# Kernel tuning notes

Hardware: AMD Instinct MI355X
Metric: run time of the kernel (lower is better)

Reference implementation:

```python
import jax, jax.numpy as jnp
import numpy as np

TOLX = 1e-12
TOLFUN = 1e-06
MAXITER = 1000
ALPHA = 1e-4
MIN_LAMBDA = 0.1
MAX_LAMBDA = 0.5
MAX_STEPS = 10  # fixed unroll budget; Newton converges in < 10 iterations for this problem
BS, NY = 200000, 8


def setup_inputs():
    key = jax.random.key(0)
    k1, k2, k3 = jax.random.split(key, 3)
    y0 = jax.random.normal(k1, (BS, NY), dtype=jnp.float32)
    W = 0.1 * jax.random.normal(k2, (NY, NY), dtype=jnp.float32)
    V = 0.1 * jax.random.normal(k3, (NY, NY), dtype=jnp.float32)
    dt = jnp.asarray(0.1, dtype=jnp.float32)
    t = jnp.asarray(1.0, dtype=jnp.float32)
    return {"y0": y0, "dt": dt, "t": t, "W": W, "V": V}


def _safe_div(n, d, eps=1e-30):
    ok = jnp.abs(d) > eps
    return jnp.where(ok, n / jnp.where(ok, d, 1.0), 0.0)


def _solver(y0, dt, t, W, V):
    bs, ny = y0.shape
    one = jnp.float32(1.0)

    def delta_S(tt, y):
        # test ODE right-hand side g(t, y): mildly nonlinear, acts per-sample
        return jnp.tanh(y @ W) @ V - 0.1 * y + 0.01 * jnp.sin(tt)

    def err(y):  # implicit-Euler residual, (bs, ny)
        return (y - y0) / dt - delta_S(t, y)

    def _err_single(yb, y0b):
        return (yb - y0b) / dt - (jnp.tanh(yb @ W) @ V - 0.1 * yb + 0.01 * jnp.sin(t))

    def batched_jac(y):
        # (bs, ny, ny): d err_b / d y_b; matches torch batch-diagonal of autograd jacobian
        return jax.vmap(jax.jacfwd(_err_single), in_axes=(0, 0))(y, y0)

    F0 = err(y0)
    jac0 = batched_jac(y0)
    rn0 = jnp.max(jnp.abs(F0), axis=1)
    fobj0 = jnp.einsum('bi,bi->b', F0, F0)

    state0 = dict(y=y0, yold=y0, F=F0, dy=jnp.zeros_like(y0), jac=jac0,
                  resnorm=rn0, resnorm0=100.0 * rn0,
                  lam=one, lam1=one, lam2=jnp.float32(0.5),
                  fold=fobj0, f2=fobj0, slope=jnp.zeros((bs,), y0.dtype),
                  lam_min=jnp.float32(0.0), niter=jnp.int32(0), exitflag=jnp.int32(1))

    def body(s, _):
        active = (((jnp.max(s['resnorm']) > TOLFUN) | (s['lam'] < 1.0))
                  & (s['exitflag'] >= 0) & (s['niter'] <= MAXITER))

        # --- lam == 1: fresh Newton direction, slope, objective ---
        is_newton = s['lam'] == 1.0
        recompute = jnp.max(_safe_div(s['resnorm'], s['resnorm0'])) > 0.2
        fresh_jac = batched_jac(s['y'])
        jac = jnp.where(is_newton & recompute, fresh_jac, s['jac'])
        dy_n = -jnp.linalg.solve(jac, s['F'][..., None])[..., 0]  # lstsq on square == solve
        gvec = jnp.einsum('bi,bij->bj', s['F'], jac)
        slope_n = jnp.einsum('bj,bj->b', gvec, dy_n)
        fold_n = jnp.einsum('bi,bi->b', s['F'], s['F'])
        lam_min_n = _safe_div(jnp.float32(TOLX),
                              jnp.max(jnp.abs(dy_n) / jnp.maximum(jnp.abs(s['y']), 1.0)))

        dy = jnp.where(is_newton, dy_n, s['dy'])
        slope = jnp.where(is_newton, slope_n, s['slope'])
        fold = jnp.where(is_newton, fold_n, s['fold'])
        yold = jnp.where(is_newton, s['y'], s['yold'])
        lam_min = jnp.where(is_newton, lam_min_n, s['lam_min'])
        niter = jnp.where(is_newton, s['niter'] + 1, s['niter'])

        brk = s['lam'] < lam_min            # -> exitflag = 2, freeze state
        bad = ~jnp.all(jnp.isfinite(dy))    # -> exitflag = -1, freeze state

        # --- trial step + trust-region line search ---
        lam = s['lam']
        y_new = yold + dy * lam
        F_new = err(y_new)
        f_obj = jnp.einsum('bi,bi->b', F_new, F_new)
        lam1 = lam
        lam2, f2 = s['lam2'], s['f2']

        backtrack = jnp.any(f_obj > fold + ALPHA * lam * slope)
        # quadratic model (first backtrack)
        lam_quad = jnp.min(_safe_div(-slope / 2.0, f_obj - fold - slope))
        # cubic model (subsequent backtracks)
        A = _safe_div(one, lam1 - lam2)
        inv1 = _safe_div(one, lam1 * lam1)
        inv2 = _safe_div(one, lam2 * lam2)
        B = jnp.stack([jnp.stack([inv1, -inv2]), jnp.stack([-lam2 * inv1, lam1 * inv2])])
        C = jnp.stack([f_obj - fold - lam1 * slope, f2 - fold - lam2 * slope])  # (2, bs)
        ab = A * (B @ C)
        a, b = ab[0], ab[1]
        disc = b * b - 3.0 * a * slope
        sq = jnp.sqrt(jnp.maximum(disc, 0.0))
        lam_tmp = jnp.where(jnp.all(a == 0.0), _safe_div(-slope, 2.0 * b),
                   jnp.where(jnp.any(disc < 0.0), MAX_LAMBDA * lam1,
                    jnp.where(jnp.any(b <= 0.0), _safe_div(-b + sq, 3.0 * a),
                     _safe_div(-slope, b + sq))))
        lam_cubic = jnp.min(jnp.minimum(lam_tmp, MAX_LAMBDA * lam1))
        lam_bt = jnp.where(lam == 1.0, lam_quad, lam_cubic)
        nanf = ~jnp.all(jnp.isfinite(f_obj))
        lam_new = jnp.where(backtrack, lam_bt, jnp.where(nanf, MAX_LAMBDA * lam1, one))

        cont = lam_new < 1.0  # retry with smaller lambda next iteration (the `continue` path)
        lam2_new = jnp.where(cont, lam1, lam2)
        f2_new = jnp.where(cont, f_obj, f2)
        lam_new = jnp.where(cont, jnp.maximum(lam_new, MIN_LAMBDA * lam1), lam_new)
        resnorm_new = jnp.where(cont, s['resnorm'], jnp.max(jnp.abs(F_new), axis=1))
        resnorm0_new = jnp.where(cont, s['resnorm0'], s['resnorm'])

        upd = active & (~brk) & (~bad)
        exitflag = jnp.where(active & brk, jnp.int32(2),
                    jnp.where(active & (~brk) & bad, jnp.int32(-1), s['exitflag']))
        sel = lambda new, old: jnp.where(upd, new, old)

        ns = dict(y=sel(y_new, s['y']), yold=sel(yold, s['yold']), F=sel(F_new, s['F']),
                  dy=sel(dy, s['dy']), jac=sel(jac, s['jac']),
                  resnorm=sel(resnorm_new, s['resnorm']), resnorm0=sel(resnorm0_new, s['resnorm0']),
                  lam=sel(lam_new, s['lam']), lam1=sel(lam1, s['lam1']), lam2=sel(lam2_new, s['lam2']),
                  fold=sel(fold, s['fold']), f2=sel(f2_new, s['f2']), slope=sel(slope, s['slope']),
                  lam_min=sel(lam_min, s['lam_min']),
                  niter=jnp.where(active, niter, s['niter']), exitflag=exitflag)
        return ns, None

    sN, _ = jax.lax.scan(body, state0, None, length=MAX_STEPS)
    return sN['y'], sN['F'], sN['exitflag']


def reference(y0, dt, t, W, V):
    y, F, exitflag = _solver(y0, dt, t, W, V)
    return (y, F, exitflag)
```

## Files before the change

### kernel.cpp

```cpp
#include <hip/hip_runtime.h>

#define BSZ 200000
#define NSTEPS 10
#define TOLFUN_C 1e-6f
#define ALPHA_C 1e-4f

#define OFF_Y     ((size_t)0)
#define OFF_YOLD  ((size_t)BSZ*8)
#define OFF_F     ((size_t)BSZ*16)
#define OFF_DY    ((size_t)BSZ*24)
#define OFF_SJ    ((size_t)BSZ*32)
#define OFF_FOLD  ((size_t)BSZ*40)
#define OFF_SLOPE ((size_t)BSZ*41)
#define OFF_RESN  ((size_t)BSZ*42)
#define OFF_F2    ((size_t)BSZ*43)
#define OFF_TRN   ((size_t)BSZ*44)
#define OFF_TFO   ((size_t)BSZ*45)
#define OFF_R     ((size_t)BSZ*46)

#define RSTRIDE 64
#define NSLOT   9
#define R_TOT   (2 + NSTEPS*NSLOT)
#define KEY_MAX_IDENT 0x007FFFFFu
#define KEY_MIN_IDENT 0xFF800000u

static __device__ __forceinline__ float nanmax2(float a, float b){
    return (__builtin_isnan(a) || __builtin_isnan(b)) ? __builtin_nanf("") : fmaxf(a, b);
}
static __device__ __forceinline__ float nanmin2(float a, float b){
    return (__builtin_isnan(a) || __builtin_isnan(b)) ? __builtin_nanf("") : fminf(a, b);
}
static __device__ __forceinline__ float safe_div(float n, float d){
    return (fabsf(d) > 1e-30f) ? (n / d) : 0.0f;
}
static __device__ __forceinline__ unsigned fkey(float x){
    unsigned u = __float_as_uint(x);
    return (u & 0x80000000u) ? ~u : (u | 0x80000000u);
}
static __device__ __forceinline__ float funkey(unsigned u){
    return (u & 0x80000000u) ? __uint_as_float(u & 0x7FFFFFFFu) : __uint_as_float(~u);
}
static __device__ __forceinline__ unsigned fkey_max(float x){
    if (__builtin_isnan(x)) x = __uint_as_float(0x7FC00000u);
    return fkey(x);
}
static __device__ __forceinline__ unsigned fkey_min(float x){
    if (__builtin_isnan(x)) x = __uint_as_float(0xFFC00000u);
    return fkey(x);
}
static __device__ __forceinline__ void ld8(const float* p, float* v){
    float4 a = ((const float4*)p)[0], b = ((const float4*)p)[1];
    v[0]=a.x; v[1]=a.y; v[2]=a.z; v[3]=a.w; v[4]=b.x; v[5]=b.y; v[6]=b.z; v[7]=b.w;
}
static __device__ __forceinline__ void st8(float* p, const float* v){
    float4 a, b;
    a.x=v[0]; a.y=v[1]; a.z=v[2]; a.w=v[3];
    b.x=v[4]; b.y=v[5]; b.z=v[6]; b.w=v[7];
    ((float4*)p)[0]=a; ((float4*)p)[1]=b;
}

struct ScalarState {
    float lam, lam1, lam2, lam_min, maxrn, ratmax;
    int   niter, exitflag;
    bool  upd_prev, cont_prev;
};

static __device__ ScalarState replay(const unsigned* R, int nsteps_done){
    ScalarState s;
    s.lam = 1.0f; s.lam1 = 1.0f; s.lam2 = 0.5f; s.lam_min = 0.0f;
    s.maxrn  = funkey(R[0]);
    s.ratmax = funkey(R[(size_t)1*RSTRIDE]);
    s.niter = 0; s.exitflag = 1;
    s.upd_prev = false; s.cont_prev = false;
    for (int j = 0; j < nsteps_done; ++j){
        const unsigned* r = R + (size_t)(2 + j*NSLOT)*RSTRIDE;
        bool active    = ((s.maxrn > TOLFUN_C) || (s.lam < 1.0f)) && (s.exitflag >= 0) && (s.niter <= 1000);
        bool is_newton = (s.lam == 1.0f);
        float lam_min_new = is_newton ? safe_div(1e-12f, funkey(r[0])) : s.lam_min;
        bool brk = (s.lam < lam_min_new);
        bool bad = is_newton ? (r[(size_t)1*RSTRIDE] != 0u) : false;
        bool upd = active && !brk && !bad;
        int niter_new = active ? (is_newton ? s.niter + 1 : s.niter) : s.niter;
        int ef_new = s.exitflag;
        if (active && brk) ef_new = 2;
        else if (active && !brk && bad) ef_new = -1;
        bool cont = false;
        if (upd){
            float lam1c = s.lam;
            unsigned bm = r[(size_t)8*RSTRIDE];
            bool backtrack = (bm & 1u) != 0u;
            float lamq  = funkey(r[(size_t)2*RSTRIDE]);
            bool allA0  = (bm & 2u) == 0u;
            bool anyDN  = (bm & 4u) != 0u;
            bool anyB0  = (bm & 8u) != 0u;
            float lam_tmp_min = allA0 ? funkey(r[(size_t)3*RSTRIDE])
                              : (anyDN ? (0.5f*lam1c)
                              : (anyB0 ? funkey(r[(size_t)4*RSTRIDE]) : funkey(r[(size_t)5*RSTRIDE])));
            float lam_cubic = nanmin2(lam_tmp_min, 0.5f*lam1c);
            float lam_bt = (s.lam == 1.0f) ? lamq : lam_cubic;
            bool nanf = (bm & 16u) != 0u;
            float lam_new = backtrack ? lam_bt : (nanf ? 0.5f*lam1c : 1.0f);
            cont = (lam_new < 1.0f);
            float lam2_new = cont ? lam1c : s.lam2;
            if (cont) lam_new = nanmax2(lam_new, 0.1f*lam1c);
            float maxrn_new  = cont ? s.maxrn  : funkey(r[(size_t)6*RSTRIDE]);
            float ratmax_new = cont ? s.ratmax : funkey(r[(size_t)7*RSTRIDE]);
            s.lam = lam_new; s.lam1 = lam1c; s.lam2 = lam2_new;
            s.lam_min = lam_min_new; s.maxrn = maxrn_new; s.ratmax = ratmax_new;
        }
        s.niter = niter_new; s.exitflag = ef_new;
        s.upd_prev = upd; s.cont_prev = cont;
    }
    return s;
}

__global__ void kPre(unsigned* __restrict__ R){
    int i = threadIdx.x;
    if (i >= R_TOT) return;
    unsigned v;
    if (i < 2) v = KEY_MAX_IDENT;
    else {
        int off = (i - 2) % NSLOT;
        bool ismin = (off==2 || off==3 || off==4 || off==5);
        bool ismax = (off==0 || off==6 || off==7);
        v = ismin ? KEY_MIN_IDENT : (ismax ? KEY_MAX_IDENT : 0u);
    }
    R[(size_t)i*RSTRIDE] = v;
}

__global__ __launch_bounds__(256) void kInit(
    const float* __restrict__ y0g, const float* __restrict__ Wm, const float* __restrict__ Vm,
    const float* __restrict__ dtp, const float* __restrict__ tp, float* __restrict__ ws)
{
    __shared__ float sW[64], sV[64];
    __shared__ float bred[2][4];
    int t = threadIdx.x;
    if (t < 64) sW[t] = Wm[t];
    else if (t < 128) sV[t-64] = Vm[t-64];
    __syncthreads();
    unsigned* R = (unsigned*)(ws + OFF_R);
    int tid = blockIdx.x*256 + t;
    bool valid = tid < BSZ;
    float c0 = 0.01f * sinf(*tp);
    float rn = -__builtin_inff(), ratio = -__builtin_inff();
    if (valid){
        float y[8]; ld8(y0g + (size_t)tid*8, y);
        float u[8], z[8], sj[8];
        #pragma unroll
        for (int k=0;k<8;k++){
            float acc = 0.f;
            #pragma unroll
            for (int m=0;m<8;m++) acc += y[m]*sW[m*8+k];
            u[k]=acc;
        }
        #pragma unroll
        for (int k=0;k<8;k++){ z[k]=tanhf(u[k]); sj[k]=1.0f - z[k]*z[k]; }
        float Fn[8];
        #pragma unroll
        for (int i=0;i<8;i++){
            float tv = 0.f;
            #pragma unroll
            for (int k=0;k<8;k++) tv += z[k]*sV[k*8+i];
            Fn[i] = 0.0f - ((tv - 0.1f*y[i]) + c0);
        }
        float fold = 0.f;
        #pragma unroll
        for (int i=0;i<8;i++) fold += Fn[i]*Fn[i];
        float rn0 = fabsf(Fn[0]);
        #pragma unroll
        for (int i=1;i<8;i++) rn0 = nanmax2(rn0, fabsf(Fn[i]));
        float zero8[8] = {0,0,0,0,0,0,0,0};
        st8(ws+OFF_Y   +(size_t)tid*8, y);
        st8(ws+OFF_YOLD+(size_t)tid*8, y);
        st8(ws+OFF_F   +(size_t)tid*8, Fn);
        st8(ws+OFF_DY  +(size_t)tid*8, zero8);
        st8(ws+OFF_SJ  +(size_t)tid*8, sj);
        ws[OFF_FOLD+tid]=fold; ws[OFF_SLOPE+tid]=0.0f;
        ws[OFF_RESN+tid]=rn0;  ws[OFF_F2+tid]=fold;
        ws[OFF_TRN+tid]=0.0f;  ws[OFF_TFO+tid]=0.0f;
        rn = rn0;
        ratio = safe_div(rn0, 100.0f*rn0);
    }
    #pragma unroll
    for (int o=32;o>=1;o>>=1){
        rn    = nanmax2(rn,    __shfl_xor(rn,    o, 64));
        ratio = nanmax2(ratio, __shfl_xor(ratio, o, 64));
    }
    int w = t >> 6;
    if ((t & 63) == 0){ bred[0][w] = rn; bred[1][w] = ratio; }
    __syncthreads();
    if (t == 0){
        float a = nanmax2(nanmax2(bred[0][0],bred[0][1]), nanmax2(bred[0][2],bred[0][3]));
        atomicMax(&R[0], fkey_max(a));
    } else if (t == 1){
        float b = nanmax2(nanmax2(bred[1][0],bred[1][1]), nanmax2(bred[1][2],bred[1][3]));
        atomicMax(&R[(size_t)1*RSTRIDE], fkey_max(b));
    }
}

__global__ __launch_bounds__(256) void phaseA(
    const float* __restrict__ Wm, const float* __restrict__ Vm,
    const float* __restrict__ dtp, float* __restrict__ ws, int step)
{
    __shared__ float sW[64], sV[64];
    __shared__ float ared[4];
    __shared__ unsigned abred[4];
    int t = threadIdx.x;
    if (t < 64) sW[t] = Wm[t];
    else if (t < 128) sV[t-64] = Vm[t-64];
    __syncthreads();

    unsigned* R = (unsigned*)(ws + OFF_R);
    ScalarState S = replay(R, step-1);
    bool active    = ((S.maxrn > TOLFUN_C) || (S.lam < 1.0f)) && (S.exitflag >= 0) && (S.niter <= 1000);
    bool is_newton = (S.lam == 1.0f);
    if (!active || !is_newton) return;
    bool recompute = (S.ratmax > 0.2f);

    int tid = blockIdx.x*256 + t;
    bool valid = tid < BSZ;
    float invdt = 1.0f / (*dtp);
    float gml = -__builtin_inff();
    bool nf = false;

    if (valid){
        float y[8], Fv[8], sj[8];
        ld8(ws+OFF_Y+(size_t)tid*8, y);
        ld8(ws+OFF_F+(size_t)tid*8, Fv);
        if (recompute){
            float u[8];
            #pragma unroll
            for (int k=0;k<8;k++){
                float acc = 0.f;
                #pragma unroll
                for (int m=0;m<8;m++) acc += y[m]*sW[m*8+k];
                u[k]=acc;
            }
            #pragma unroll
            for (int k=0;k<8;k++){ float z = tanhf(u[k]); sj[k] = 1.0f - z*z; }
            st8(ws+OFF_SJ+(size_t)tid*8, sj);
        } else {
            ld8(ws+OFF_SJ+(size_t)tid*8, sj);
        }
        float J[8][8];
        #pragma unroll
        for (int j=0;j<8;j++){
            float zj[8];
            #pragma unroll
            for (int k=0;k<8;k++) zj[k] = sW[j*8+k]*sj[k];
            #pragma unroll
            for (int i=0;i<8;i++){
                float acc = 0.f;
                #pragma unroll
                for (int k=0;k<8;k++) acc += zj[k]*sV[k*8+i];
                J[i][j] = (i==j) ? (invdt - (acc - 0.1f)) : (0.0f - acc);
            }
        }
        float fold = 0.f;
        #pragma unroll
        for (int i=0;i<8;i++) fold += Fv[i]*Fv[i];
        float gv[8];
        #pragma unroll
        for (int j=0;j<8;j++){
            float acc = 0.f;
            #pragma unroll
            for (int i=0;i<8;i++) acc += Fv[i]*J[i][j];
            gv[j]=acc;
        }
        float x[8];
        #pragma unroll
        for (int i=0;i<8;i++) x[i]=Fv[i];
        #pragma unroll
        for (int c=0;c<8;c++){
            float ip = 1.0f / J[c][c];
            #pragma unroll
            for (int r2=c+1;r2<8;r2++){
                float m = J[r2][c]*ip;
                #pragma unroll
                for (int jj=c+1;jj<8;jj++) J[r2][jj] -= m*J[c][jj];
                x[r2] -= m*x[c];
            }
        }
        float wv[8];
        #pragma unroll
        for (int c=7;c>=0;c--){
            float acc = x[c];
            #pragma unroll
            for (int jj=c+1;jj<8;jj++) acc -= J[c][jj]*wv[jj];
            wv[c] = acc / J[c][c];
        }
        float dy[8];
        #pragma unroll
        for (int i=0;i<8;i++) dy[i] = -wv[i];
        float slope = 0.f;
        #pragma unroll
        for (int j=0;j<8;j++) slope += gv[j]*dy[j];
        st8(ws+OFF_DY  +(size_t)tid*8, dy);
        st8(ws+OFF_YOLD+(size_t)tid*8, y);
        ws[OFF_FOLD+tid]  = fold;
        ws[OFF_SLOPE+tid] = slope;
        #pragma unroll
        for (int i=0;i<8;i++){
            float rr = fabsf(dy[i]) / nanmax2(fabsf(y[i]), 1.0f);
            gml = nanmax2(gml, rr);
            nf = nf || !__builtin_isfinite(dy[i]);
        }
    }
    #pragma unroll
    for (int o=32;o>=1;o>>=1) gml = nanmax2(gml, __shfl_xor(gml, o, 64));
    unsigned long long anym = __ballot(nf ? 1 : 0);
    int w = t >> 6;
    if ((t & 63) == 0){ ared[w] = gml; abred[w] = anym ? 1u : 0u; }
    __syncthreads();
    unsigned* r1 = R + (size_t)(2 + (step-1)*NSLOT)*RSTRIDE;
    if (t == 0){
        float v = nanmax2(nanmax2(ared[0],ared[1]), nanmax2(ared[2],ared[3]));
        atomicMax(&r1[0], fkey_max(v));
    } else if (t == 1){
        unsigned bm = abred[0]|abred[1]|abred[2]|abred[3];
        if (bm) atomicOr(&r1[(size_t)1*RSTRIDE], 1u);
    }
}

__global__ __launch_bounds__(256) void phaseB(
    const float* __restrict__ y0g, const float* __restrict__ Wm, const float* __restrict__ Vm,
    const float* __restrict__ dtp, const float* __restrict__ tp,
    float* __restrict__ ws, int step)
{
    __shared__ float sW[64], sV[64];
    __shared__ float fred[6][4];
    __shared__ unsigned bbred[4];
    int t = threadIdx.x;
    if (t < 64) sW[t] = Wm[t];
    else if (t < 128) sV[t-64] = Vm[t-64];
    __syncthreads();

    unsigned* R = (unsigned*)(ws + OFF_R);
    ScalarState S = replay(R, step-1);
    bool active    = ((S.maxrn > TOLFUN_C) || (S.lam < 1.0f)) && (S.exitflag >= 0) && (S.niter <= 1000);
    bool is_newton = (S.lam == 1.0f);
    unsigned* r = R + (size_t)(2 + (step-1)*NSLOT)*RSTRIDE;
    float lam_min_new = is_newton ? safe_div(1e-12f, funkey(r[0])) : S.lam_min;
    bool brk = (S.lam < lam_min_new);
    bool bad = is_newton ? (r[(size_t)1*RSTRIDE] != 0u) : false;
    bool upd = active && !brk && !bad;
    if (!upd) return;

    int tid = blockIdx.x*256 + t;
    bool valid = tid < BSZ;
    float dt = *dtp;
    float c0 = 0.01f * sinf(*tp);
    float lam = S.lam, lam2 = S.lam2;

    bool armijo=false, aNot0=false, dN=false, ble=false, nanf=false;
    float lq = __builtin_inff(), mX = __builtin_inff(), mZ = __builtin_inff(), mW = __builtin_inff();
    float trn = -__builtin_inff(), ratio = -__builtin_inff();

    if (valid){
        float f2v   = ws[OFF_F2+tid];
        float rnold = ws[OFF_RESN+tid];
        if (S.upd_prev){
            if (S.cont_prev){ f2v = ws[OFF_TFO+tid]; ws[OFF_F2+tid] = f2v; }
            else            { rnold = ws[OFF_TRN+tid]; ws[OFF_RESN+tid] = rnold; }
        }
        float foldv  = ws[OFF_FOLD+tid];
        float slopev = ws[OFF_SLOPE+tid];
        float yold[8], dyv[8];
        ld8(ws+OFF_YOLD+(size_t)tid*8, yold);
        ld8(ws+OFF_DY  +(size_t)tid*8, dyv);
        float yn[8];
        #pragma unroll
        for (int i=0;i<8;i++) yn[i] = yold[i] + dyv[i]*lam;
        float u[8], z[8];
        #pragma unroll
        for (int k=0;k<8;k++){
            float acc = 0.f;
            #pragma unroll
            for (int m=0;m<8;m++) acc += yn[m]*sW[m*8+k];
            u[k]=acc;
        }
        #pragma unroll
        for (int k=0;k<8;k++) z[k] = tanhf(u[k]);
        float Fn[8];
        #pragma unroll
        for (int i=0;i<8;i++){
            float tv = 0.f;
            #pragma unroll
            for (int k=0;k<8;k++) tv += z[k]*sV[k*8+i];
            Fn[i] = (yn[i] - y0g[(size_t)tid*8+i])/dt - ((tv - 0.1f*yn[i]) + c0);
        }
        float f_obj = 0.f;
        #pragma unroll
        for (int i=0;i<8;i++) f_obj += Fn[i]*Fn[i];
        st8(ws+OFF_Y+(size_t)tid*8, yn);
        st8(ws+OFF_F+(size_t)tid*8, Fn);
        float rn = fabsf(Fn[0]);
        #pragma unroll
        for (int i=1;i<8;i++) rn = nanmax2(rn, fabsf(Fn[i]));
        ws[OFF_TRN+tid] = rn;
        ws[OFF_TFO+tid] = f_obj;

        armijo = f_obj > (foldv + (ALPHA_C*lam)*slopev);
        lq = safe_div((-slopev)*0.5f, (f_obj - foldv) - slopev);
        float lam1v = lam;
        float Af = safe_div(1.0f, lam1v - lam2);
        float i1 = safe_div(1.0f, lam1v*lam1v);
        float i2 = safe_div(1.0f, lam2*lam2);
        float Cc0 = (f_obj - foldv) - lam1v*slopev;
        float Cc1 = (f2v  - foldv) - lam2 *slopev;
        float av = Af*(i1*Cc0 - i2*Cc1);
        float bv = Af*((-(lam2*i1))*Cc0 + (lam1v*i2)*Cc1);
        float disc = bv*bv - (3.0f*av)*slopev;
        float dm = __builtin_isnan(disc) ? disc : fmaxf(disc, 0.0f);
        float sq = sqrtf(dm);
        aNot0 = (av != 0.0f);
        dN    = (disc < 0.0f);
        ble   = (bv <= 0.0f);
        mX = safe_div(-slopev, 2.0f*bv);
        mZ = safe_div(-bv + sq, 3.0f*av);
        mW = safe_div(-slopev, bv + sq);
        nanf = !__builtin_isfinite(f_obj);
        trn = rn;
        ratio = safe_div(rn, rnold);
    }
    #pragma unroll
    for (int o=32;o>=1;o>>=1){
        lq    = nanmin2(lq,    __shfl_xor(lq,    o, 64));
        mX    = nanmin2(mX,    __shfl_xor(mX,    o, 64));
        mZ    = nanmin2(mZ,    __shfl_xor(mZ,    o, 64));
        mW    = nanmin2(mW,    __shfl_xor(mW,    o, 64));
        trn   = nanmax2(trn,   __shfl_xor(trn,   o, 64));
        ratio = nanmax2(ratio, __shfl_xor(ratio, o, 64));
    }
    unsigned long long bArm = __ballot(armijo ? 1 : 0);
    unsigned long long bA0  = __ballot(aNot0  ? 1 : 0);
    unsigned long long bDN  = __ballot(dN     ? 1 : 0);
    unsigned long long bB0  = __ballot(ble    ? 1 : 0);
    unsigned long long bNF  = __ballot(nanf   ? 1 : 0);
    int w = t >> 6;
    if ((t & 63) == 0){
        fred[0][w]=lq; fred[1][w]=mX; fred[2][w]=mZ; fred[3][w]=mW;
        fred[4][w]=trn; fred[5][w]=ratio;
        bbred[w] = (bArm?1u:0u) | (bA0?2u:0u) | (bDN?4u:0u) | (bB0?8u:0u) | (bNF?16u:0u);
    }
    __syncthreads();
    if (t < 6){
        float v = fred[t][0];
        bool ismin = (t < 4);
        #pragma unroll
        for (int w2=1; w2<4; ++w2) v = ismin ? nanmin2(v, fred[t][w2]) : nanmax2(v, fred[t][w2]);
        unsigned* p = &r[(size_t)(t + 2)*RSTRIDE];
        if (ismin) atomicMin(p, fkey_min(v));
        else       atomicMax(p, fkey_max(v));
    } else if (t == 6){
        unsigned bm = bbred[0]|bbred[1]|bbred[2]|bbred[3];
        if (bm) atomicOr(&r[(size_t)8*RSTRIDE], bm);
    }
}

__global__ __launch_bounds__(256) void kOut(const float* __restrict__ ws, float* __restrict__ out)
{
    const unsigned* R = (const unsigned*)(ws + OFF_R);
    ScalarState S = replay(R, NSTEPS);
    int tid = blockIdx.x*256 + threadIdx.x;
    if (tid < BSZ){
        float v[8];
        ld8(ws+OFF_Y+(size_t)tid*8, v);
        st8(out + (size_t)tid*8, v);
        ld8(ws+OFF_F+(size_t)tid*8, v);
        st8(out + (size_t)BSZ*8 + (size_t)tid*8, v);
    }
    if (tid == 0) out[(size_t)BSZ*16] = (float)S.exitflag;
}

extern "C" void kernel_launch(void* const* d_in, const int* in_sizes, int n_in,
                              void* d_out, int out_size, void* d_ws, size_t ws_size,
                              hipStream_t stream)
{
    const float* y0g = (const float*)d_in[0];
    const float* dtp = (const float*)d_in[1];
    const float* tp  = (const float*)d_in[2];
    const float* Wm  = (const float*)d_in[3];
    const float* Vm  = (const float*)d_in[4];
    float* ws  = (float*)d_ws;
    float* out = (float*)d_out;
    dim3 grid((BSZ + 255)/256), blk(256);

    hipLaunchKernelGGL(kPre, dim3(1), dim3(128), 0, stream, (unsigned*)(ws + OFF_R));
    hipLaunchKernelGGL(kInit, grid, blk, 0, stream, y0g, Wm, Vm, dtp, tp, ws);
    for (int s = 1; s <= NSTEPS; ++s){
        hipLaunchKernelGGL(phaseA, grid, blk, 0, stream, Wm, Vm, dtp, ws, s);
        hipLaunchKernelGGL(phaseB, grid, blk, 0, stream, y0g, Wm, Vm, dtp, tp, ws, s);
    }
    hipLaunchKernelGGL(kOut, grid, blk, 0, stream, ws, out);
}
```

Measured before the change: 459.4 us.

## Fuse Newton solver into one persistent cooperative kernel with grid syncs

Replaces the 22-launch sequence (init, phaseA/phaseB per step, output) with a single cooperative kernel. Per-sample state stays in registers across all steps, and the cross-sample reductions use global atomics with grid.sync between phases. F is recomputed at the end instead of being stored every step. This removes per-launch overhead and the global-memory round trips of per-sample state. In exchange it risks high register pressure, since each thread holds two samples' state plus an 8x8 Jacobian, and it depends on cooperative launch support, with a multi-kernel fallback if that launch fails.

Measured after the change: 569.1 us. 1.24x slower.

```diff
diff --git a/kernel.cpp b/kernel.cpp
--- a/kernel.cpp
+++ b/kernel.cpp
@@ -1,22 +1,32 @@
 #include <hip/hip_runtime.h>
+#include <hip/hip_cooperative_groups.h>
+
+namespace cg = cooperative_groups;
 
 #define BSZ 200000
 #define NSTEPS 10
 #define TOLFUN_C 1e-6f
 #define ALPHA_C 1e-4f
 
+#define CNTHR 512
+#define CNBLK 256
+#define CNT   (CNBLK*CNTHR)
+#define SPT   2
+
+#define FNTHR 256
+#define FNBLK ((BSZ + FNTHR - 1)/FNTHR)
+
 #define OFF_Y     ((size_t)0)
 #define OFF_YOLD  ((size_t)BSZ*8)
-#define OFF_F     ((size_t)BSZ*16)
-#define OFF_DY    ((size_t)BSZ*24)
-#define OFF_SJ    ((size_t)BSZ*32)
-#define OFF_FOLD  ((size_t)BSZ*40)
-#define OFF_SLOPE ((size_t)BSZ*41)
-#define OFF_RESN  ((size_t)BSZ*42)
-#define OFF_F2    ((size_t)BSZ*43)
-#define OFF_TRN   ((size_t)BSZ*44)
-#define OFF_TFO   ((size_t)BSZ*45)
-#define OFF_R     ((size_t)BSZ*46)
+#define OFF_DY    ((size_t)BSZ*16)
+#define OFF_SJ    ((size_t)BSZ*24)
+#define OFF_FOLD  ((size_t)BSZ*32)
+#define OFF_SLOPE ((size_t)BSZ*33)
+#define OFF_RESN  ((size_t)BSZ*34)
+#define OFF_F2    ((size_t)BSZ*35)
+#define OFF_TFO   ((size_t)BSZ*36)
+#define OFF_TRN   ((size_t)BSZ*37)
+#define OFF_R     ((size_t)BSZ*38)
 
 #define RSTRIDE 64
 #define NSLOT   9
@@ -58,6 +68,181 @@
     b.x=v[4]; b.y=v[5]; b.z=v[6]; b.w=v[7];
     ((float4*)p)[0]=a; ((float4*)p)[1]=b;
 }
+static __device__ __forceinline__ unsigned ldslot(const unsigned* p){
+    return __hip_atomic_load(p, __ATOMIC_RELAXED, __HIP_MEMORY_SCOPE_AGENT);
+}
+static __device__ __forceinline__ void stslot(unsigned* p, unsigned v){
+    __hip_atomic_store(p, v, __ATOMIC_RELAXED, __HIP_MEMORY_SCOPE_AGENT);
+}
+
+struct Smp {
+    float y0[8], y[8], yold[8], dy[8], sj[8];
+    float fold, slope, resn, f2, tfo, trn;
+};
+
+static __device__ __forceinline__ void computeFz(
+    const float* yv, const float* y0v, float dt, float c0,
+    const float* sW, const float* sV, float* Fo, float* zo)
+{
+    float u[8];
+    #pragma unroll
+    for (int k=0;k<8;k++){
+        float acc = 0.f;
+        #pragma unroll
+        for (int m=0;m<8;m++) acc += yv[m]*sW[m*8+k];
+        u[k]=acc;
+    }
+    #pragma unroll
+    for (int k=0;k<8;k++) zo[k] = tanhf(u[k]);
+    #pragma unroll
+    for (int i=0;i<8;i++){
+        float tv = 0.f;
+        #pragma unroll
+        for (int k=0;k<8;k++) tv += zo[k]*sV[k*8+i];
+        Fo[i] = (yv[i]-y0v[i])/dt - ((tv - 0.1f*yv[i]) + c0);
+    }
+}
+
+static __device__ __forceinline__ void devInit(Smp& s, float dt, float c0,
+    const float* sW, const float* sV, float& rn_red, float& rat_red)
+{
+    #pragma unroll
+    for (int i=0;i<8;i++){ s.y[i]=s.y0[i]; s.yold[i]=s.y0[i]; s.dy[i]=0.f; }
+    float Fv[8], z[8];
+    computeFz(s.y, s.y0, dt, c0, sW, sV, Fv, z);
+    #pragma unroll
+    for (int k=0;k<8;k++) s.sj[k] = 1.0f - z[k]*z[k];
+    float fold = 0.f;
+    #pragma unroll
+    for (int i=0;i<8;i++) fold += Fv[i]*Fv[i];
+    float rn0 = fabsf(Fv[0]);
+    #pragma unroll
+    for (int i=1;i<8;i++) rn0 = nanmax2(rn0, fabsf(Fv[i]));
+    s.fold=fold; s.slope=0.f; s.resn=rn0; s.f2=fold; s.tfo=0.f; s.trn=0.f;
+    rn_red  = nanmax2(rn_red, rn0);
+    rat_red = nanmax2(rat_red, safe_div(rn0, 100.0f*rn0));
+}
+
+static __device__ __forceinline__ void devA(Smp& s, float dt, float invdt, float c0,
+    const float* sW, const float* sV, bool recompute, float& gml, bool& nf)
+{
+    float Fv[8], z[8];
+    computeFz(s.y, s.y0, dt, c0, sW, sV, Fv, z);
+    if (recompute){
+        #pragma unroll
+        for (int k=0;k<8;k++) s.sj[k] = 1.0f - z[k]*z[k];
+    }
+    float J[8][8];
+    #pragma unroll
+    for (int j=0;j<8;j++){
+        float zj[8];
+        #pragma unroll
+        for (int k=0;k<8;k++) zj[k] = sW[j*8+k]*s.sj[k];
+        #pragma unroll
+        for (int i=0;i<8;i++){
+            float acc = 0.f;
+            #pragma unroll
+            for (int k=0;k<8;k++) acc += zj[k]*sV[k*8+i];
+            J[i][j] = (i==j) ? (invdt - (acc - 0.1f)) : (0.0f - acc);
+        }
+    }
+    float fold = 0.f;
+    #pragma unroll
+    for (int i=0;i<8;i++) fold += Fv[i]*Fv[i];
+    float gv[8];
+    #pragma unroll
+    for (int j=0;j<8;j++){
+        float acc = 0.f;
+        #pragma unroll
+        for (int i=0;i<8;i++) acc += Fv[i]*J[i][j];
+        gv[j]=acc;
+    }
+    float x[8];
+    #pragma unroll
+    for (int i=0;i<8;i++) x[i]=Fv[i];
+    #pragma unroll
+    for (int c=0;c<8;c++){
+        float ip = 1.0f / J[c][c];
+        #pragma unroll
+        for (int r2=c+1;r2<8;r2++){
+            float m = J[r2][c]*ip;
+            #pragma unroll
+            for (int jj=c+1;jj<8;jj++) J[r2][jj] -= m*J[c][jj];
+            x[r2] -= m*x[c];
+        }
+    }
+    float wv[8];
+    #pragma unroll
+    for (int c=7;c>=0;c--){
+        float acc = x[c];
+        #pragma unroll
+        for (int jj=c+1;jj<8;jj++) acc -= J[c][jj]*wv[jj];
+        wv[c] = acc / J[c][c];
+    }
+    #pragma unroll
+    for (int i=0;i<8;i++){
+        s.yold[i] = s.y[i];
+        s.dy[i]   = -wv[i];
+    }
+    float slope = 0.f;
+    #pragma unroll
+    for (int j=0;j<8;j++) slope += gv[j]*s.dy[j];
+    s.fold = fold; s.slope = slope;
+    #pragma unroll
+    for (int i=0;i<8;i++){
+        float rr = fabsf(s.dy[i]) / nanmax2(fabsf(s.y[i]), 1.0f);
+        gml = nanmax2(gml, rr);
+        nf = nf || !__builtin_isfinite(s.dy[i]);
+    }
+}
+
+static __device__ __forceinline__ void devB(Smp& s, float dt, float c0,
+    const float* sW, const float* sV, float lam, float lam2v,
+    bool& armijo, float& lq, bool& aNot0, bool& dN, bool& ble,
+    float& mX, float& mZ, float& mW, bool& nanf, float& trnR, float& ratR)
+{
+    float yn[8];
+    #pragma unroll
+    for (int i=0;i<8;i++) yn[i] = s.yold[i] + s.dy[i]*lam;
+    float Ft[8], z[8];
+    computeFz(yn, s.y0, dt, c0, sW, sV, Ft, z);
+    float f_obj = 0.f;
+    #pragma unroll
+    for (int i=0;i<8;i++) f_obj += Ft[i]*Ft[i];
+    float rn = fabsf(Ft[0]);
+    #pragma unroll
+    for (int i=1;i<8;i++) rn = nanmax2(rn, fabsf(Ft[i]));
+    s.tfo = f_obj; s.trn = rn;
+    armijo = armijo || (f_obj > (s.fold + (ALPHA_C*lam)*s.slope));
+    lq = nanmin2(lq, safe_div((-s.slope)*0.5f, (f_obj - s.fold) - s.slope));
+    float lam1v = lam;
+    float Af = safe_div(1.0f, lam1v - lam2v);
+    float i1 = safe_div(1.0f, lam1v*lam1v);
+    float i2 = safe_div(1.0f, lam2v*lam2v);
+    float Cc0 = (f_obj - s.fold) - lam1v*s.slope;
+    float Cc1 = (s.f2  - s.fold) - lam2v*s.slope;
+    float av = Af*(i1*Cc0 - i2*Cc1);
+    float bv = Af*((-(lam2v*i1))*Cc0 + (lam1v*i2)*Cc1);
+    float disc = bv*bv - (3.0f*av)*s.slope;
+    float dm = __builtin_isnan(disc) ? disc : fmaxf(disc, 0.0f);
+    float sq = sqrtf(dm);
+    aNot0 = aNot0 || (av != 0.0f);
+    dN    = dN    || (disc < 0.0f);
+    ble   = ble   || (bv <= 0.0f);
+    mX = nanmin2(mX, safe_div(-s.slope, 2.0f*bv));
+    mZ = nanmin2(mZ, safe_div(-bv + sq, 3.0f*av));
+    mW = nanmin2(mW, safe_div(-s.slope, bv + sq));
+    nanf = nanf || !__builtin_isfinite(f_obj);
+    trnR = nanmax2(trnR, rn);
+    ratR = nanmax2(ratR, safe_div(rn, s.resn));
+}
+
+static __device__ __forceinline__ void devCommit(Smp& s, float lam1, bool cont){
+    #pragma unroll
+    for (int i=0;i<8;i++) s.y[i] = s.yold[i] + s.dy[i]*lam1;
+    if (cont) s.f2 = s.tfo;
+    else      s.resn = s.trn;
+}
 
 struct ScalarState {
     float lam, lam1, lam2, lam_min, maxrn, ratmax;
@@ -65,53 +250,238 @@
     bool  upd_prev, cont_prev;
 };
 
-static __device__ ScalarState replay(const unsigned* R, int nsteps_done){
+static __device__ void advance(ScalarState& s, const unsigned* R, int j){
+    const unsigned* r = R + (size_t)(2 + j*NSLOT)*RSTRIDE;
+    unsigned v0 = ldslot(r + (size_t)0*RSTRIDE);
+    unsigned v1 = ldslot(r + (size_t)1*RSTRIDE);
+    unsigned v2 = ldslot(r + (size_t)2*RSTRIDE);
+    unsigned v3 = ldslot(r + (size_t)3*RSTRIDE);
+    unsigned v4 = ldslot(r + (size_t)4*RSTRIDE);
+    unsigned v5 = ldslot(r + (size_t)5*RSTRIDE);
+    unsigned v6 = ldslot(r + (size_t)6*RSTRIDE);
+    unsigned v7 = ldslot(r + (size_t)7*RSTRIDE);
+    unsigned v8 = ldslot(r + (size_t)8*RSTRIDE);
+    bool active    = ((s.maxrn > TOLFUN_C) || (s.lam < 1.0f)) && (s.exitflag >= 0) && (s.niter <= 1000);
+    bool is_newton = (s.lam == 1.0f);
+    float lam_min_new = is_newton ? safe_div(1e-12f, funkey(v0)) : s.lam_min;
+    bool brk = (s.lam < lam_min_new);
+    bool bad = is_newton ? (v1 != 0u) : false;
+    bool upd = active && !brk && !bad;
+    int niter_new = active ? (is_newton ? s.niter + 1 : s.niter) : s.niter;
+    int ef_new = s.exitflag;
+    if (active && brk) ef_new = 2;
+    else if (active && !brk && bad) ef_new = -1;
+    bool cont = false;
+    if (upd){
+        float lam1c = s.lam;
+        unsigned bm = v8;
+        bool backtrack = (bm & 1u) != 0u;
+        float lamq  = funkey(v2);
+        bool allA0  = (bm & 2u) == 0u;
+        bool anyDN  = (bm & 4u) != 0u;
+        bool anyB0  = (bm & 8u) != 0u;
+        float lam_tmp_min = allA0 ? funkey(v3)
+                          : (anyDN ? (0.5f*lam1c)
+                          : (anyB0 ? funkey(v4) : funkey(v5)));
+        float lam_cubic = nanmin2(lam_tmp_min, 0.5f*lam1c);
+        float lam_bt = (s.lam == 1.0f) ? lamq : lam_cubic;
+        bool nanf = (bm & 16u) != 0u;
+        float lam_new = backtrack ? lam_bt : (nanf ? 0.5f*lam1c : 1.0f);
+        cont = (lam_new < 1.0f);
+        float lam2_new = cont ? lam1c : s.lam2;
+        if (cont) lam_new = nanmax2(lam_new, 0.1f*lam1c);
+        float maxrn_new  = cont ? s.maxrn  : funkey(v6);
+        float ratmax_new = cont ? s.ratmax : funkey(v7);
+        s.lam = lam_new; s.lam1 = lam1c; s.lam2 = lam2_new;
+        s.lam_min = lam_min_new; s.maxrn = maxrn_new; s.ratmax = ratmax_new;
+    }
+    s.niter = niter_new; s.exitflag = ef_new;
+    s.upd_prev = upd; s.cont_prev = cont;
+}
+
+static __device__ ScalarState replayN(const unsigned* R, int n){
     ScalarState s;
-    s.lam = 1.0f; s.lam1 = 1.0f; s.lam2 = 0.5f; s.lam_min = 0.0f;
-    s.maxrn  = funkey(R[0]);
-    s.ratmax = funkey(R[(size_t)1*RSTRIDE]);
-    s.niter = 0; s.exitflag = 1;
-    s.upd_prev = false; s.cont_prev = false;
-    for (int j = 0; j < nsteps_done; ++j){
-        const unsigned* r = R + (size_t)(2 + j*NSLOT)*RSTRIDE;
-        bool active    = ((s.maxrn > TOLFUN_C) || (s.lam < 1.0f)) && (s.exitflag >= 0) && (s.niter <= 1000);
-        bool is_newton = (s.lam == 1.0f);
-        float lam_min_new = is_newton ? safe_div(1e-12f, funkey(r[0])) : s.lam_min;
-        bool brk = (s.lam < lam_min_new);
-        bool bad = is_newton ? (r[(size_t)1*RSTRIDE] != 0u) : false;
-        bool upd = active && !brk && !bad;
-        int niter_new = active ? (is_newton ? s.niter + 1 : s.niter) : s.niter;
-        int ef_new = s.exitflag;
-        if (active && brk) ef_new = 2;
-        else if (active && !brk && bad) ef_new = -1;
-        bool cont = false;
-        if (upd){
-            float lam1c = s.lam;
-            unsigned bm = r[(size_t)8*RSTRIDE];
-            bool backtrack = (bm & 1u) != 0u;
-            float lamq  = funkey(r[(size_t)2*RSTRIDE]);
-            bool allA0  = (bm & 2u) == 0u;
-            bool anyDN  = (bm & 4u) != 0u;
-            bool anyB0  = (bm & 8u) != 0u;
-            float lam_tmp_min = allA0 ? funkey(r[(size_t)3*RSTRIDE])
-                              : (anyDN ? (0.5f*lam1c)
-                              : (anyB0 ? funkey(r[(size_t)4*RSTRIDE]) : funkey(r[(size_t)5*RSTRIDE])));
-            float lam_cubic = nanmin2(lam_tmp_min, 0.5f*lam1c);
-            float lam_bt = (s.lam == 1.0f) ? lamq : lam_cubic;
-            bool nanf = (bm & 16u) != 0u;
-            float lam_new = backtrack ? lam_bt : (nanf ? 0.5f*lam1c : 1.0f);
-            cont = (lam_new < 1.0f);
-            float lam2_new = cont ? lam1c : s.lam2;
-            if (cont) lam_new = nanmax2(lam_new, 0.1f*lam1c);
-            float maxrn_new  = cont ? s.maxrn  : funkey(r[(size_t)6*RSTRIDE]);
-            float ratmax_new = cont ? s.ratmax : funkey(r[(size_t)7*RSTRIDE]);
-            s.lam = lam_new; s.lam1 = lam1c; s.lam2 = lam2_new;
-            s.lam_min = lam_min_new; s.maxrn = maxrn_new; s.ratmax = ratmax_new;
-        }
-        s.niter = niter_new; s.exitflag = ef_new;
-        s.upd_prev = upd; s.cont_prev = cont;
-    }
+    s.lam=1.0f; s.lam1=1.0f; s.lam2=0.5f; s.lam_min=0.0f;
+    s.maxrn  = funkey(ldslot(&R[0]));
+    s.ratmax = funkey(ldslot(&R[(size_t)1*RSTRIDE]));
+    s.niter=0; s.exitflag=1; s.upd_prev=false; s.cont_prev=false;
+    for (int j=0;j<n;++j) advance(s, R, j);
     return s;
+}
+
+__global__ __launch_bounds__(CNTHR, 2) void kFused(
+    const float* __restrict__ y0g, const float* __restrict__ Wm, const float* __restrict__ Vm,
+    const float* __restrict__ dtp, const float* __restrict__ tp,
+    float* __restrict__ ws, float* __restrict__ out)
+{
+    cg::grid_group gridg = cg::this_grid();
+    __shared__ float sW[64], sV[64];
+    __shared__ float redF[6][8];
+    __shared__ unsigned redB[8];
+    int t = threadIdx.x;
+    if (t < 64) sW[t] = Wm[t];
+    else if (t < 128) sV[t-64] = Vm[t-64];
+    unsigned* R = (unsigned*)(ws + OFF_R);
+    if (blockIdx.x == 0 && t < R_TOT){
+        unsigned v;
+        if (t < 2) v = KEY_MAX_IDENT;
+        else {
+            int off = (t - 2) % NSLOT;
+            bool ismin = (off==2 || off==3 || off==4 || off==5);
+            bool ismax = (off==0 || off==6 || off==7);
+            v = ismin ? KEY_MIN_IDENT : (ismax ? KEY_MAX_IDENT : 0u);
+        }
+        stslot(&R[(size_t)t*RSTRIDE], v);
+    }
+    __syncthreads();
+    gridg.sync();
+
+    int gtid = blockIdx.x*CNTHR + t;
+    float dt = *dtp, invdt = 1.0f/dt, c0 = 0.01f*sinf(*tp);
+
+    Smp s[SPT]; bool valid[SPT];
+    float rn_red = -__builtin_inff(), rat_red = -__builtin_inff();
+    #pragma unroll
+    for (int q=0;q<SPT;q++){
+        int sid = gtid + q*CNT;
+        valid[q] = sid < BSZ;
+        if (valid[q]){
+            ld8(y0g + (size_t)sid*8, s[q].y0);
+            devInit(s[q], dt, c0, sW, sV, rn_red, rat_red);
+        } else {
+            #pragma unroll
+            for (int i=0;i<8;i++){ s[q].y0[i]=0; s[q].y[i]=0; s[q].yold[i]=0; s[q].dy[i]=0; s[q].sj[i]=0; }
+            s[q].fold=0; s[q].slope=0; s[q].resn=0; s[q].f2=0; s[q].tfo=0; s[q].trn=0;
+        }
+    }
+    #pragma unroll
+    for (int o=32;o>=1;o>>=1){
+        rn_red  = nanmax2(rn_red,  __shfl_xor(rn_red,  o, 64));
+        rat_red = nanmax2(rat_red, __shfl_xor(rat_red, o, 64));
+    }
+    {
+        int w = t >> 6;
+        if ((t & 63) == 0){ redF[0][w] = rn_red; redF[1][w] = rat_red; }
+        __syncthreads();
+        if (t == 0){
+            float a = redF[0][0];
+            #pragma unroll
+            for (int w2=1;w2<8;w2++) a = nanmax2(a, redF[0][w2]);
+            atomicMax(&R[0], fkey_max(a));
+        } else if (t == 1){
+            float b = redF[1][0];
+            #pragma unroll
+            for (int w2=1;w2<8;w2++) b = nanmax2(b, redF[1][w2]);
+            atomicMax(&R[(size_t)1*RSTRIDE], fkey_max(b));
+        }
+    }
+    gridg.sync();
+
+    ScalarState S;
+    S.lam=1.0f; S.lam1=1.0f; S.lam2=0.5f; S.lam_min=0.0f;
+    S.maxrn  = funkey(ldslot(&R[0]));
+    S.ratmax = funkey(ldslot(&R[(size_t)1*RSTRIDE]));
+    S.niter=0; S.exitflag=1; S.upd_prev=false; S.cont_prev=false;
+
+    #pragma unroll 1
+    for (int k=1; k<=NSTEPS; ++k){
+        if (S.upd_prev){
+            #pragma unroll
+            for (int q=0;q<SPT;q++) if (valid[q]) devCommit(s[q], S.lam1, S.cont_prev);
+        }
+        bool active    = ((S.maxrn > TOLFUN_C) || (S.lam < 1.0f)) && (S.exitflag >= 0) && (S.niter <= 1000);
+        bool is_newton = (S.lam == 1.0f);
+        unsigned* r = R + (size_t)(2 + (k-1)*NSLOT)*RSTRIDE;
+
+        if (active && is_newton){
+            bool recompute = (S.ratmax > 0.2f);
+            float gml = -__builtin_inff(); bool nf = false;
+            #pragma unroll
+            for (int q=0;q<SPT;q++) if (valid[q]) devA(s[q], dt, invdt, c0, sW, sV, recompute, gml, nf);
+            #pragma unroll
+            for (int o=32;o>=1;o>>=1) gml = nanmax2(gml, __shfl_xor(gml, o, 64));
+            unsigned long long anym = __ballot(nf ? 1 : 0);
+            int w = t >> 6;
+            if ((t & 63) == 0){ redF[0][w] = gml; redB[w] = anym ? 1u : 0u; }
+            __syncthreads();
+            if (t == 0){
+                float v = redF[0][0];
+                #pragma unroll
+                for (int w2=1;w2<8;w2++) v = nanmax2(v, redF[0][w2]);
+                atomicMax(&r[0], fkey_max(v));
+            } else if (t == 1){
+                unsigned bm = 0u;
+                #pragma unroll
+                for (int w2=0;w2<8;w2++) bm |= redB[w2];
+                if (bm) atomicOr(&r[(size_t)1*RSTRIDE], 1u);
+            }
+            __syncthreads();
+        }
+
+        if (active){
+            float lam = S.lam, lam2v = S.lam2;
+            bool armijo=false, aNot0=false, dN=false, ble=false, nanf=false;
+            float lq=__builtin_inff(), mX=__builtin_inff(), mZ=__builtin_inff(), mW=__builtin_inff();
+            float trnR=-__builtin_inff(), ratR=-__builtin_inff();
+            #pragma unroll
+            for (int q=0;q<SPT;q++)
+                if (valid[q]) devB(s[q], dt, c0, sW, sV, lam, lam2v,
+                                   armijo, lq, aNot0, dN, ble, mX, mZ, mW, nanf, trnR, ratR);
+            #pragma unroll
+            for (int o=32;o>=1;o>>=1){
+                lq   = nanmin2(lq,   __shfl_xor(lq,   o, 64));
+                mX   = nanmin2(mX,   __shfl_xor(mX,   o, 64));
+                mZ   = nanmin2(mZ,   __shfl_xor(mZ,   o, 64));
+                mW   = nanmin2(mW,   __shfl_xor(mW,   o, 64));
+                trnR = nanmax2(trnR, __shfl_xor(trnR, o, 64));
+                ratR = nanmax2(ratR, __shfl_xor(ratR, o, 64));
+            }
+            unsigned long long bArm = __ballot(armijo ? 1 : 0);
+            unsigned long long bA0  = __ballot(aNot0  ? 1 : 0);
+            unsigned long long bDN  = __ballot(dN     ? 1 : 0);
+            unsigned long long bB0  = __ballot(ble    ? 1 : 0);
+            unsigned long long bNF  = __ballot(nanf   ? 1 : 0);
+            int w = t >> 6;
+            if ((t & 63) == 0){
+                redF[0][w]=lq; redF[1][w]=mX; redF[2][w]=mZ; redF[3][w]=mW;
+                redF[4][w]=trnR; redF[5][w]=ratR;
+                redB[w] = (bArm?1u:0u) | (bA0?2u:0u) | (bDN?4u:0u) | (bB0?8u:0u) | (bNF?16u:0u);
+            }
+            __syncthreads();
+            if (t < 6){
+                float v = redF[t][0];
+                bool ismin = (t < 4);
+                #pragma unroll
+                for (int w2=1;w2<8;w2++) v = ismin ? nanmin2(v, redF[t][w2]) : nanmax2(v, redF[t][w2]);
+                unsigned* p = &r[(size_t)(t + 2)*RSTRIDE];
+                if (ismin) atomicMin(p, fkey_min(v));
+                else       atomicMax(p, fkey_max(v));
+            } else if (t == 6){
+                unsigned bm = 0u;
+                #pragma unroll
+                for (int w2=0;w2<8;w2++) bm |= redB[w2];
+                if (bm) atomicOr(&r[(size_t)8*RSTRIDE], bm);
+            }
+        }
+
+        gridg.sync();
+        advance(S, R, k-1);
+    }
+
+    if (S.upd_prev){
+        #pragma unroll
+        for (int q=0;q<SPT;q++) if (valid[q]) devCommit(s[q], S.lam1, S.cont_prev);
+    }
+    #pragma unroll
+    for (int q=0;q<SPT;q++){
+        if (!valid[q]) continue;
+        int sid = gtid + q*CNT;
+        st8(out + (size_t)sid*8, s[q].y);
+        float Fv[8], z[8];
+        computeFz(s[q].y, s[q].y0, dt, c0, sW, sV, Fv, z);
+        st8(out + (size_t)BSZ*8 + (size_t)sid*8, Fv);
+    }
+    if (gtid == 0) out[(size_t)BSZ*16] = (float)S.exitflag;
 }
 
 __global__ void kPre(unsigned* __restrict__ R){
@@ -128,349 +498,206 @@
     R[(size_t)i*RSTRIDE] = v;
 }
 
-__global__ __launch_bounds__(256) void kInit(
+static __device__ __forceinline__ void storeSmp(float* ws, int tid, const Smp& s){
+    st8(ws+OFF_Y   +(size_t)tid*8, s.y);
+    st8(ws+OFF_YOLD+(size_t)tid*8, s.yold);
+    st8(ws+OFF_DY  +(size_t)tid*8, s.dy);
+    st8(ws+OFF_SJ  +(size_t)tid*8, s.sj);
+    ws[OFF_FOLD+tid]=s.fold; ws[OFF_SLOPE+tid]=s.slope;
+    ws[OFF_RESN+tid]=s.resn; ws[OFF_F2+tid]=s.f2;
+    ws[OFF_TFO+tid]=s.tfo;   ws[OFF_TRN+tid]=s.trn;
+}
+static __device__ __forceinline__ void loadSmp(const float* ws, int tid, Smp& s){
+    ld8(ws+OFF_Y   +(size_t)tid*8, s.y);
+    ld8(ws+OFF_YOLD+(size_t)tid*8, s.yold);
+    ld8(ws+OFF_DY  +(size_t)tid*8, s.dy);
+    ld8(ws+OFF_SJ  +(size_t)tid*8, s.sj);
+    s.fold=ws[OFF_FOLD+tid]; s.slope=ws[OFF_SLOPE+tid];
+    s.resn=ws[OFF_RESN+tid]; s.f2=ws[OFF_F2+tid];
+    s.tfo=ws[OFF_TFO+tid];   s.trn=ws[OFF_TRN+tid];
+}
+
+__global__ __launch_bounds__(FNTHR) void fInit(
     const float* __restrict__ y0g, const float* __restrict__ Wm, const float* __restrict__ Vm,
     const float* __restrict__ dtp, const float* __restrict__ tp, float* __restrict__ ws)
 {
     __shared__ float sW[64], sV[64];
-    __shared__ float bred[2][4];
+    __shared__ float red[2][4];
     int t = threadIdx.x;
     if (t < 64) sW[t] = Wm[t];
     else if (t < 128) sV[t-64] = Vm[t-64];
     __syncthreads();
     unsigned* R = (unsigned*)(ws + OFF_R);
-    int tid = blockIdx.x*256 + t;
+    int tid = blockIdx.x*FNTHR + t;
     bool valid = tid < BSZ;
-    float c0 = 0.01f * sinf(*tp);
-    float rn = -__builtin_inff(), ratio = -__builtin_inff();
+    float dt = *dtp, c0 = 0.01f*sinf(*tp);
+    float rn_red = -__builtin_inff(), rat_red = -__builtin_inff();
     if (valid){
-        float y[8]; ld8(y0g + (size_t)tid*8, y);
-        float u[8], z[8], sj[8];
-        #pragma unroll
-        for (int k=0;k<8;k++){
-            float acc = 0.f;
-            #pragma unroll
-            for (int m=0;m<8;m++) acc += y[m]*sW[m*8+k];
-            u[k]=acc;
-        }
-        #pragma unroll
-        for (int k=0;k<8;k++){ z[k]=tanhf(u[k]); sj[k]=1.0f - z[k]*z[k]; }
-        float Fn[8];
-        #pragma unroll
-        for (int i=0;i<8;i++){
-            float tv = 0.f;
-            #pragma unroll
-            for (int k=0;k<8;k++) tv += z[k]*sV[k*8+i];
-            Fn[i] = 0.0f - ((tv - 0.1f*y[i]) + c0);
-        }
-        float fold = 0.f;
-        #pragma unroll
-        for (int i=0;i<8;i++) fold += Fn[i]*Fn[i];
-        float rn0 = fabsf(Fn[0]);
-        #pragma unroll
-        for (int i=1;i<8;i++) rn0 = nanmax2(rn0, fabsf(Fn[i]));
-        float zero8[8] = {0,0,0,0,0,0,0,0};
-        st8(ws+OFF_Y   +(size_t)tid*8, y);
-        st8(ws+OFF_YOLD+(size_t)tid*8, y);
-        st8(ws+OFF_F   +(size_t)tid*8, Fn);
-        st8(ws+OFF_DY  +(size_t)tid*8, zero8);
-        st8(ws+OFF_SJ  +(size_t)tid*8, sj);
-        ws[OFF_FOLD+tid]=fold; ws[OFF_SLOPE+tid]=0.0f;
-        ws[OFF_RESN+tid]=rn0;  ws[OFF_F2+tid]=fold;
-        ws[OFF_TRN+tid]=0.0f;  ws[OFF_TFO+tid]=0.0f;
-        rn = rn0;
-        ratio = safe_div(rn0, 100.0f*rn0);
+        Smp s;
+        ld8(y0g + (size_t)tid*8, s.y0);
+        devInit(s, dt, c0, sW, sV, rn_red, rat_red);
+        storeSmp(ws, tid, s);
     }
     #pragma unroll
     for (int o=32;o>=1;o>>=1){
-        rn    = nanmax2(rn,    __shfl_xor(rn,    o, 64));
-        ratio = nanmax2(ratio, __shfl_xor(ratio, o, 64));
+        rn_red  = nanmax2(rn_red,  __shfl_xor(rn_red,  o, 64));
+        rat_red = nanmax2(rat_red, __shfl_xor(rat_red, o, 64));
     }
     int w = t >> 6;
-    if ((t & 63) == 0){ bred[0][w] = rn; bred[1][w] = ratio; }
+    if ((t & 63) == 0){ red[0][w]=rn_red; red[1][w]=rat_red; }
     __syncthreads();
     if (t == 0){
-        float a = nanmax2(nanmax2(bred[0][0],bred[0][1]), nanmax2(bred[0][2],bred[0][3]));
+        float a = red[0][0];
+        for (int w2=1;w2<4;w2++) a = nanmax2(a, red[0][w2]);
         atomicMax(&R[0], fkey_max(a));
     } else if (t == 1){
-        float b = nanmax2(nanmax2(bred[1][0],bred[1][1]), nanmax2(bred[1][2],bred[1][3]));
+        float b = red[1][0];
+        for (int w2=1;w2<4;w2++) b = nanmax2(b, red[1][w2]);
         atomicMax(&R[(size_t)1*RSTRIDE], fkey_max(b));
     }
 }
 
-__global__ __launch_bounds__(256) void phaseA(
-    const float* __restrict__ Wm, const float* __restrict__ Vm,
-    const float* __restrict__ dtp, float* __restrict__ ws, int step)
+__global__ __launch_bounds__(FNTHR) void fStep(
+    const float* __restrict__ y0g, const float* __restrict__ Wm, const float* __restrict__ Vm,
+    const float* __restrict__ dtp, const float* __restrict__ tp,
+    float* __restrict__ ws, int step)
 {
     __shared__ float sW[64], sV[64];
-    __shared__ float ared[4];
-    __shared__ unsigned abred[4];
+    __shared__ float redF[6][4];
+    __shared__ unsigned redB[4];
     int t = threadIdx.x;
     if (t < 64) sW[t] = Wm[t];
     else if (t < 128) sV[t-64] = Vm[t-64];
     __syncthreads();
-
     unsigned* R = (unsigned*)(ws + OFF_R);
-    ScalarState S = replay(R, step-1);
+    ScalarState S = replayN(R, step-1);
     bool active    = ((S.maxrn > TOLFUN_C) || (S.lam < 1.0f)) && (S.exitflag >= 0) && (S.niter <= 1000);
     bool is_newton = (S.lam == 1.0f);
-    if (!active || !is_newton) return;
-    bool recompute = (S.ratmax > 0.2f);
-
-    int tid = blockIdx.x*256 + t;
+    if (!S.upd_prev && !active) return;
+
+    int tid = blockIdx.x*FNTHR + t;
     bool valid = tid < BSZ;
-    float invdt = 1.0f / (*dtp);
-    float gml = -__builtin_inff();
-    bool nf = false;
-
+    float dt = *dtp, invdt = 1.0f/dt, c0 = 0.01f*sinf(*tp);
+    unsigned* r = R + (size_t)(2 + (step-1)*NSLOT)*RSTRIDE;
+
+    Smp s;
     if (valid){
-        float y[8], Fv[8], sj[8];
-        ld8(ws+OFF_Y+(size_t)tid*8, y);
-        ld8(ws+OFF_F+(size_t)tid*8, Fv);
-        if (recompute){
-            float u[8];
-            #pragma unroll
-            for (int k=0;k<8;k++){
-                float acc = 0.f;
-                #pragma unroll
-                for (int m=0;m<8;m++) acc += y[m]*sW[m*8+k];
-                u[k]=acc;
-            }
-            #pragma unroll
-            for (int k=0;k<8;k++){ float z = tanhf(u[k]); sj[k] = 1.0f - z*z; }
-            st8(ws+OFF_SJ+(size_t)tid*8, sj);
-        } else {
-            ld8(ws+OFF_SJ+(size_t)tid*8, sj);
-        }
-        float J[8][8];
-        #pragma unroll
-        for (int j=0;j<8;j++){
-            float zj[8];
-            #pragma unroll
-            for (int k=0;k<8;k++) zj[k] = sW[j*8+k]*sj[k];
-            #pragma unroll
-            for (int i=0;i<8;i++){
-                float acc = 0.f;
-                #pragma unroll
-                for (int k=0;k<8;k++) acc += zj[k]*sV[k*8+i];
-                J[i][j] = (i==j) ? (invdt - (acc - 0.1f)) : (0.0f - acc);
-            }
-        }
-        float fold = 0.f;
-        #pragma unroll
-        for (int i=0;i<8;i++) fold += Fv[i]*Fv[i];
-        float gv[8];
-        #pragma unroll
-        for (int j=0;j<8;j++){
-            float acc = 0.f;
-            #pragma unroll
-            for (int i=0;i<8;i++) acc += Fv[i]*J[i][j];
-            gv[j]=acc;
-        }
-        float x[8];
-        #pragma unroll
-        for (int i=0;i<8;i++) x[i]=Fv[i];
-        #pragma unroll
-        for (int c=0;c<8;c++){
-            float ip = 1.0f / J[c][c];
-            #pragma unroll
-            for (int r2=c+1;r2<8;r2++){
-                float m = J[r2][c]*ip;
-                #pragma unroll
-                for (int jj=c+1;jj<8;jj++) J[r2][jj] -= m*J[c][jj];
-                x[r2] -= m*x[c];
-            }
-        }
-        float wv[8];
-        #pragma unroll
-        for (int c=7;c>=0;c--){
-            float acc = x[c];
-            #pragma unroll
-            for (int jj=c+1;jj<8;jj++) acc -= J[c][jj]*wv[jj];
-            wv[c] = acc / J[c][c];
-        }
-        float dy[8];
-        #pragma unroll
-        for (int i=0;i<8;i++) dy[i] = -wv[i];
-        float slope = 0.f;
-        #pragma unroll
-        for (int j=0;j<8;j++) slope += gv[j]*dy[j];
-        st8(ws+OFF_DY  +(size_t)tid*8, dy);
-        st8(ws+OFF_YOLD+(size_t)tid*8, y);
-        ws[OFF_FOLD+tid]  = fold;
-        ws[OFF_SLOPE+tid] = slope;
-        #pragma unroll
-        for (int i=0;i<8;i++){
-            float rr = fabsf(dy[i]) / nanmax2(fabsf(y[i]), 1.0f);
-            gml = nanmax2(gml, rr);
-            nf = nf || !__builtin_isfinite(dy[i]);
-        }
-    }
-    #pragma unroll
-    for (int o=32;o>=1;o>>=1) gml = nanmax2(gml, __shfl_xor(gml, o, 64));
-    unsigned long long anym = __ballot(nf ? 1 : 0);
-    int w = t >> 6;
-    if ((t & 63) == 0){ ared[w] = gml; abred[w] = anym ? 1u : 0u; }
-    __syncthreads();
-    unsigned* r1 = R + (size_t)(2 + (step-1)*NSLOT)*RSTRIDE;
-    if (t == 0){
-        float v = nanmax2(nanmax2(ared[0],ared[1]), nanmax2(ared[2],ared[3]));
-        atomicMax(&r1[0], fkey_max(v));
-    } else if (t == 1){
-        unsigned bm = abred[0]|abred[1]|abred[2]|abred[3];
-        if (bm) atomicOr(&r1[(size_t)1*RSTRIDE], 1u);
-    }
-}
-
-__global__ __launch_bounds__(256) void phaseB(
+        ld8(y0g + (size_t)tid*8, s.y0);
+        loadSmp(ws, tid, s);
+        if (S.upd_prev){
+            devCommit(s, S.lam1, S.cont_prev);
+            st8(ws+OFF_Y+(size_t)tid*8, s.y);
+            if (S.cont_prev) ws[OFF_F2+tid]   = s.f2;
+            else             ws[OFF_RESN+tid] = s.resn;
+        }
+    }
+    if (!active) return;
+
+    if (is_newton){
+        bool recompute = (S.ratmax > 0.2f);
+        float gml = -__builtin_inff(); bool nf = false;
+        if (valid){
+            devA(s, dt, invdt, c0, sW, sV, recompute, gml, nf);
+            st8(ws+OFF_YOLD+(size_t)tid*8, s.yold);
+            st8(ws+OFF_DY  +(size_t)tid*8, s.dy);
+            if (recompute) st8(ws+OFF_SJ+(size_t)tid*8, s.sj);
+            ws[OFF_FOLD+tid]  = s.fold;
+            ws[OFF_SLOPE+tid] = s.slope;
+        }
+        #pragma unroll
+        for (int o=32;o>=1;o>>=1) gml = nanmax2(gml, __shfl_xor(gml, o, 64));
+        unsigned long long anym = __ballot(nf ? 1 : 0);
+        int w = t >> 6;
+        if ((t & 63) == 0){ redF[0][w] = gml; redB[w] = anym ? 1u : 0u; }
+        __syncthreads();
+        if (t == 0){
+            float v = redF[0][0];
+            for (int w2=1;w2<4;w2++) v = nanmax2(v, redF[0][w2]);
+            atomicMax(&r[0], fkey_max(v));
+        } else if (t == 1){
+            unsigned bm = redB[0]|redB[1]|redB[2]|redB[3];
+            if (bm) atomicOr(&r[(size_t)1*RSTRIDE], 1u);
+        }
+        __syncthreads();
+    }
+
+    {
+        float lam = S.lam, lam2v = S.lam2;
+        bool armijo=false, aNot0=false, dN=false, ble=false, nanf=false;
+        float lq=__builtin_inff(), mX=__builtin_inff(), mZ=__builtin_inff(), mW=__builtin_inff();
+        float trnR=-__builtin_inff(), ratR=-__builtin_inff();
+        if (valid){
+            devB(s, dt, c0, sW, sV, lam, lam2v,
+                 armijo, lq, aNot0, dN, ble, mX, mZ, mW, nanf, trnR, ratR);
+            ws[OFF_TFO+tid] = s.tfo;
+            ws[OFF_TRN+tid] = s.trn;
+        }
+        #pragma unroll
+        for (int o=32;o>=1;o>>=1){
+            lq   = nanmin2(lq,   __shfl_xor(lq,   o, 64));
+            mX   = nanmin2(mX,   __shfl_xor(mX,   o, 64));
+            mZ   = nanmin2(mZ,   __shfl_xor(mZ,   o, 64));
+            mW   = nanmin2(mW,   __shfl_xor(mW,   o, 64));
+            trnR = nanmax2(trnR, __shfl_xor(trnR, o, 64));
+            ratR = nanmax2(ratR, __shfl_xor(ratR, o, 64));
+        }
+        unsigned long long bArm = __ballot(armijo ? 1 : 0);
+        unsigned long long bA0  = __ballot(aNot0  ? 1 : 0);
+        unsigned long long bDN  = __ballot(dN     ? 1 : 0);
+        unsigned long long bB0  = __ballot(ble    ? 1 : 0);
+        unsigned long long bNF  = __ballot(nanf   ? 1 : 0);
+        int w = t >> 6;
+        if ((t & 63) == 0){
+            redF[0][w]=lq; redF[1][w]=mX; redF[2][w]=mZ; redF[3][w]=mW;
+            redF[4][w]=trnR; redF[5][w]=ratR;
+            redB[w] = (bArm?1u:0u) | (bA0?2u:0u) | (bDN?4u:0u) | (bB0?8u:0u) | (bNF?16u:0u);
+        }
+        __syncthreads();
+        if (t < 6){
+            float v = redF[t][0];
+            bool ismin = (t < 4);
+            for (int w2=1;w2<4;w2++) v = ismin ? nanmin2(v, redF[t][w2]) : nanmax2(v, redF[t][w2]);
+            unsigned* p = &r[(size_t)(t + 2)*RSTRIDE];
+            if (ismin) atomicMin(p, fkey_min(v));
+            else       atomicMax(p, fkey_max(v));
+        } else if (t == 6){
+            unsigned bm = redB[0]|redB[1]|redB[2]|redB[3];
+            if (bm) atomicOr(&r[(size_t)8*RSTRIDE], bm);
+        }
+    }
+}
+
+__global__ __launch_bounds__(FNTHR) void fOut(
     const float* __restrict__ y0g, const float* __restrict__ Wm, const float* __restrict__ Vm,
     const float* __restrict__ dtp, const float* __restrict__ tp,
-    float* __restrict__ ws, int step)
+    const float* __restrict__ ws, float* __restrict__ out)
 {
     __shared__ float sW[64], sV[64];
-    __shared__ float fred[6][4];
-    __shared__ unsigned bbred[4];
     int t = threadIdx.x;
     if (t < 64) sW[t] = Wm[t];
     else if (t < 128) sV[t-64] = Vm[t-64];
     __syncthreads();
-
-    unsigned* R = (unsigned*)(ws + OFF_R);
-    ScalarState S = replay(R, step-1);
-    bool active    = ((S.maxrn > TOLFUN_C) || (S.lam < 1.0f)) && (S.exitflag >= 0) && (S.niter <= 1000);
-    bool is_newton = (S.lam == 1.0f);
-    unsigned* r = R + (size_t)(2 + (step-1)*NSLOT)*RSTRIDE;
-    float lam_min_new = is_newton ? safe_div(1e-12f, funkey(r[0])) : S.lam_min;
-    bool brk = (S.lam < lam_min_new);
-    bool bad = is_newton ? (r[(size_t)1*RSTRIDE] != 0u) : false;
-    bool upd = active && !brk && !bad;
-    if (!upd) return;
-
-    int tid = blockIdx.x*256 + t;
-    bool valid = tid < BSZ;
-    float dt = *dtp;
-    float c0 = 0.01f * sinf(*tp);
-    float lam = S.lam, lam2 = S.lam2;
-
-    bool armijo=false, aNot0=false, dN=false, ble=false, nanf=false;
-    float lq = __builtin_inff(), mX = __builtin_inff(), mZ = __builtin_inff(), mW = __builtin_inff();
-    float trn = -__builtin_inff(), ratio = -__builtin_inff();
-
-    if (valid){
-        float f2v   = ws[OFF_F2+tid];
-        float rnold = ws[OFF_RESN+tid];
+    const unsigned* R = (const unsigned*)(ws + OFF_R);
+    ScalarState S = replayN(R, NSTEPS);
+    int tid = blockIdx.x*FNTHR + t;
+    float dt = *dtp, c0 = 0.01f*sinf(*tp);
+    if (tid < BSZ){
+        float y0v[8], yv[8];
+        ld8(y0g + (size_t)tid*8, y0v);
+        ld8(ws+OFF_Y+(size_t)tid*8, yv);
         if (S.upd_prev){
-            if (S.cont_prev){ f2v = ws[OFF_TFO+tid]; ws[OFF_F2+tid] = f2v; }
-            else            { rnold = ws[OFF_TRN+tid]; ws[OFF_RESN+tid] = rnold; }
-        }
-        float foldv  = ws[OFF_FOLD+tid];
-        float slopev = ws[OFF_SLOPE+tid];
-        float yold[8], dyv[8];
-        ld8(ws+OFF_YOLD+(size_t)tid*8, yold);
-        ld8(ws+OFF_DY  +(size_t)tid*8, dyv);
-        float yn[8];
-        #pragma unroll
-        for (int i=0;i<8;i++) yn[i] = yold[i] + dyv[i]*lam;
-        float u[8], z[8];
-        #pragma unroll
-        for (int k=0;k<8;k++){
-            float acc = 0.f;
-            #pragma unroll
-            for (int m=0;m<8;m++) acc += yn[m]*sW[m*8+k];
-            u[k]=acc;
-        }
-        #pragma unroll
-        for (int k=0;k<8;k++) z[k] = tanhf(u[k]);
-        float Fn[8];
-        #pragma unroll
-        for (int i=0;i<8;i++){
-            float tv = 0.f;
-            #pragma unroll
-            for (int k=0;k<8;k++) tv += z[k]*sV[k*8+i];
-            Fn[i] = (yn[i] - y0g[(size_t)tid*8+i])/dt - ((tv - 0.1f*yn[i]) + c0);
-        }
-        float f_obj = 0.f;
-        #pragma unroll
-        for (int i=0;i<8;i++) f_obj += Fn[i]*Fn[i];
-        st8(ws+OFF_Y+(size_t)tid*8, yn);
-        st8(ws+OFF_F+(size_t)tid*8, Fn);
-        float rn = fabsf(Fn[0]);
-        #pragma unroll
-        for (int i=1;i<8;i++) rn = nanmax2(rn, fabsf(Fn[i]));
-        ws[OFF_TRN+tid] = rn;
-        ws[OFF_TFO+tid] = f_obj;
-
-        armijo = f_obj > (foldv + (ALPHA_C*lam)*slopev);
-        lq = safe_div((-slopev)*0.5f, (f_obj - foldv) - slopev);
-        float lam1v = lam;
-        float Af = safe_div(1.0f, lam1v - lam2);
-        float i1 = safe_div(1.0f, lam1v*lam1v);
-        float i2 = safe_div(1.0f, lam2*lam2);
-        float Cc0 = (f_obj - foldv) - lam1v*slopev;
-        float Cc1 = (f2v  - foldv) - lam2 *slopev;
-        float av = Af*(i1*Cc0 - i2*Cc1);
-        float bv = Af*((-(lam2*i1))*Cc0 + (lam1v*i2)*Cc1);
-        float disc = bv*bv - (3.0f*av)*slopev;
-        float dm = __builtin_isnan(disc) ? disc : fmaxf(disc, 0.0f);
-        float sq = sqrtf(dm);
-        aNot0 = (av != 0.0f);
-        dN    = (disc < 0.0f);
-        ble   = (bv <= 0.0f);
-        mX = safe_div(-slopev, 2.0f*bv);
-        mZ = safe_div(-bv + sq, 3.0f*av);
-        mW = safe_div(-slopev, bv + sq);
-        nanf = !__builtin_isfinite(f_obj);
-        trn = rn;
-        ratio = safe_div(rn, rnold);
-    }
-    #pragma unroll
-    for (int o=32;o>=1;o>>=1){
-        lq    = nanmin2(lq,    __shfl_xor(lq,    o, 64));
-        mX    = nanmin2(mX,    __shfl_xor(mX,    o, 64));
-        mZ    = nanmin2(mZ,    __shfl_xor(mZ,    o, 64));
-        mW    = nanmin2(mW,    __shfl_xor(mW,    o, 64));
-        trn   = nanmax2(trn,   __shfl_xor(trn,   o, 64));
-        ratio = nanmax2(ratio, __shfl_xor(ratio, o, 64));
-    }
-    unsigned long long bArm = __ballot(armijo ? 1 : 0);
-    unsigned long long bA0  = __ballot(aNot0  ? 1 : 0);
-    unsigned long long bDN  = __ballot(dN     ? 1 : 0);
-    unsigned long long bB0  = __ballot(ble    ? 1 : 0);
-    unsigned long long bNF  = __ballot(nanf   ? 1 : 0);
-    int w = t >> 6;
-    if ((t & 63) == 0){
-        fred[0][w]=lq; fred[1][w]=mX; fred[2][w]=mZ; fred[3][w]=mW;
-        fred[4][w]=trn; fred[5][w]=ratio;
-        bbred[w] = (bArm?1u:0u) | (bA0?2u:0u) | (bDN?4u:0u) | (bB0?8u:0u) | (bNF?16u:0u);
-    }
-    __syncthreads();
-    if (t < 6){
-        float v = fred[t][0];
-        bool ismin = (t < 4);
-        #pragma unroll
-        for (int w2=1; w2<4; ++w2) v = ismin ? nanmin2(v, fred[t][w2]) : nanmax2(v, fred[t][w2]);
-        unsigned* p = &r[(size_t)(t + 2)*RSTRIDE];
-        if (ismin) atomicMin(p, fkey_min(v));
-        else       atomicMax(p, fkey_max(v));
-    } else if (t == 6){
-        unsigned bm = bbred[0]|bbred[1]|bbred[2]|bbred[3];
-        if (bm) atomicOr(&r[(size_t)8*RSTRIDE], bm);
-    }
-}
-
-__global__ __launch_bounds__(256) void kOut(const float* __restrict__ ws, float* __restrict__ out)
-{
-    const unsigned* R = (const unsigned*)(ws + OFF_R);
-    ScalarState S = replay(R, NSTEPS);
-    int tid = blockIdx.x*256 + threadIdx.x;
-    if (tid < BSZ){
-        float v[8];
-        ld8(ws+OFF_Y+(size_t)tid*8, v);
-        st8(out + (size_t)tid*8, v);
-        ld8(ws+OFF_F+(size_t)tid*8, v);
-        st8(out + (size_t)BSZ*8 + (size_t)tid*8, v);
-    }
-    if (tid == 0) out[(size_t)BSZ*16] = (float)S.exitflag;
+            float yo[8], dv[8];
+            ld8(ws+OFF_YOLD+(size_t)tid*8, yo);
+            ld8(ws+OFF_DY  +(size_t)tid*8, dv);
+            #pragma unroll
+            for (int i=0;i<8;i++) yv[i] = yo[i] + dv[i]*S.lam1;
+        }
+        st8(out + (size_t)tid*8, yv);
+        float Fv[8], z[8];
+        computeFz(yv, y0v, dt, c0, sW, sV, Fv, z);
+        st8(out + (size_t)BSZ*8 + (size_t)tid*8, Fv);
+    }
+    if (blockIdx.x == 0 && t == 0) out[(size_t)BSZ*16] = (float)S.exitflag;
 }
 
 extern "C" void kernel_launch(void* const* d_in, const int* in_sizes, int n_in,
@@ -482,15 +709,18 @@
     const float* tp  = (const float*)d_in[2];
     const float* Wm  = (const float*)d_in[3];
     const float* Vm  = (const float*)d_in[4];
-    float* ws  = (float*)d_ws;
-    float* out = (float*)d_out;
-    dim3 grid((BSZ + 255)/256), blk(256);
-
-    hipLaunchKernelGGL(kPre, dim3(1), dim3(128), 0, stream, (unsigned*)(ws + OFF_R));
-    hipLaunchKernelGGL(kInit, grid, blk, 0, stream, y0g, Wm, Vm, dtp, tp, ws);
-    for (int s = 1; s <= NSTEPS; ++s){
-        hipLaunchKernelGGL(phaseA, grid, blk, 0, stream, Wm, Vm, dtp, ws, s);
-        hipLaunchKernelGGL(phaseB, grid, blk, 0, stream, y0g, Wm, Vm, dtp, tp, ws, s);
-    }
-    hipLaunchKernelGGL(kOut, grid, blk, 0, stream, ws, out);
-}
+    float* ws   = (float*)d_ws;
+    float* outp = (float*)d_out;
+
+    void* args[] = {(void*)&y0g, (void*)&Wm, (void*)&Vm, (void*)&dtp, (void*)&tp,
+                    (void*)&ws, (void*)&outp};
+    hipError_t rc = hipLaunchCooperativeKernel((const void*)kFused, dim3(CNBLK), dim3(CNTHR),
+                                               args, 0, stream);
+    if (rc != hipSuccess){
+        hipLaunchKernelGGL(kPre, dim3(1), dim3(128), 0, stream, (unsigned*)(ws + OFF_R));
+        hipLaunchKernelGGL(fInit, dim3(FNBLK), dim3(FNTHR), 0, stream, y0g, Wm, Vm, dtp, tp, ws);
+        for (int s = 1; s <= NSTEPS; ++s)
+            hipLaunchKernelGGL(fStep, dim3(FNBLK), dim3(FNTHR), 0, stream, y0g, Wm, Vm, dtp, tp, ws, s);
+        hipLaunchKernelGGL(fOut, dim3(FNBLK), dim3(FNTHR), 0, stream, y0g, Wm, Vm, dtp, tp, ws, outp);
+    }
+}
```
